# Optimization experiments

Measured on AMD Instinct MI355X. Metric: run time of the kernel, lower is better.

## Reference

```python
import jax, jax.numpy as jnp
import numpy as np

TOP_K = 2


def setup_inputs() -> dict:
    key = jax.random.key(0)
    ks = jax.random.split(key, 10)
    D, F, E = 1024, 4096, 8
    s = 0.02  # realistic init scale, keeps activations stable
    return {
        "x": jax.random.normal(ks[0], (2, 4096, D), dtype=jnp.float32),
        "gate_w": jax.random.normal(ks[1], (E, D), dtype=jnp.float32) * s,
        "w1": jax.random.normal(ks[2], (E, F, D), dtype=jnp.float32) * s,
        "b1": jax.random.normal(ks[3], (E, F), dtype=jnp.float32) * s,
        "w2": jax.random.normal(ks[4], (E, D, F), dtype=jnp.float32) * s,
        "b2": jax.random.normal(ks[5], (E, D), dtype=jnp.float32) * s,
        "sw1": jax.random.normal(ks[6], (F, D), dtype=jnp.float32) * s,
        "sb1": jax.random.normal(ks[7], (F,), dtype=jnp.float32) * s,
        "sw2": jax.random.normal(ks[8], (D, F), dtype=jnp.float32) * s,
        "sb2": jax.random.normal(ks[9], (D,), dtype=jnp.float32) * s,
    }


def _ffn(x, w1, b1, w2, b2):
    # GELU(x @ W1^T + b1) @ W2^T + b2 ; torch F.gelu default = exact (erf)
    h = jax.nn.gelu(x @ w1.T + b1, approximate=False)
    return h @ w2.T + b2


def reference(x, gate_w, w1, b1, w2, b2, sw1, sb1, sw2, sb2):
    B, S, D = x.shape
    E = gate_w.shape[0]
    xt = x.reshape(-1, D)  # [T, D]

    # MoEGate: linear -> softmax -> top-k (weights not renormalized)
    scores = jax.nn.softmax(xt @ gate_w.T, axis=-1)  # [T, E]
    topk_w, topk_idx = jax.lax.top_k(scores, TOP_K)  # [T, K]

    # moe_infer: per-expert FFN, combine with top-k gate weights.
    # Reference form: dense per-expert compute, masked combine (combine sum is
    # permutation-invariant so top-k ordering does not matter).
    out = jnp.zeros_like(xt)
    for e in range(E):
        we = jnp.sum(jnp.where(topk_idx == e, topk_w, 0.0), axis=-1)  # [T]
        out = out + we[:, None] * _ffn(xt, w1[e], b1[e], w2[e], b2[e])

    # shared expert applied to the identity input
    out = out + _ffn(xt, sw1, sb1, sw2, sb2)
    return out.reshape(B, S, D)
```

## Files before the change

### kernel.cpp

```cpp
#include <hip/hip_runtime.h>
#include <hip/hip_bf16.h>

typedef __bf16 bf16_t;
typedef __bf16 bf16x8 __attribute__((ext_vector_type(8)));
typedef float  f32x4  __attribute__((ext_vector_type(4)));

static constexpr int TT = 8192;
static constexpr int DD = 1024;
static constexpr int FF = 4096;
static constexpr int NSLOT = 2 * TT;

#define R_COUNTS 0
#define R_OFFSET 8
#define R_TSTART 17
#define R_TOTAL  34
#define R_INTS   40

#define GLL(g, l) __builtin_amdgcn_global_load_lds( \
    (__attribute__((address_space(1))) void*)(g), \
    (__attribute__((address_space(3))) void*)(l), 16, 0, 0)

__device__ __forceinline__ float fast_gelu(float v) {
  float t = -1.5957691216f * v - 0.0713548162f * (v * v * v);
  return v / (1.f + __expf(t));
}

__global__ __launch_bounds__(256) void cvt_f32_bf16(const float* __restrict__ src,
                                                    bf16_t* __restrict__ dst, int n8) {
  int i = blockIdx.x * 256 + threadIdx.x;
  if (i >= n8) return;
  const float4* s = reinterpret_cast<const float4*>(src) + (size_t)i * 2;
  float4 a = s[0], b = s[1];
  bf16x8 v;
  v[0] = (bf16_t)a.x; v[1] = (bf16_t)a.y; v[2] = (bf16_t)a.z; v[3] = (bf16_t)a.w;
  v[4] = (bf16_t)b.x; v[5] = (bf16_t)b.y; v[6] = (bf16_t)b.z; v[7] = (bf16_t)b.w;
  *reinterpret_cast<bf16x8*>(dst + (size_t)i * 8) = v;
}

__global__ __launch_bounds__(256) void gate_kernel(const float* __restrict__ x,
                                                   const float* __restrict__ gw,
                                                   float* __restrict__ topkw,
                                                   int* __restrict__ slote) {
  int wid = threadIdx.x >> 6, lane = threadIdx.x & 63;
  int t = blockIdx.x * 4 + wid;
  const float4* xv = reinterpret_cast<const float4*>(x + (size_t)t * DD) + lane * 4;
  const float4* gv = reinterpret_cast<const float4*>(gw);
  float acc[8];
#pragma unroll
  for (int e = 0; e < 8; ++e) acc[e] = 0.f;
#pragma unroll
  for (int i = 0; i < 4; ++i) {
    float4 xi = xv[i];
#pragma unroll
    for (int e = 0; e < 8; ++e) {
      float4 g = gv[e * 256 + lane * 4 + i];
      acc[e] += xi.x * g.x + xi.y * g.y + xi.z * g.z + xi.w * g.w;
    }
  }
#pragma unroll
  for (int e = 0; e < 8; ++e)
    for (int off = 32; off; off >>= 1) acc[e] += __shfl_xor(acc[e], off, 64);
  if (lane == 0) {
    float m = acc[0];
#pragma unroll
    for (int e = 1; e < 8; ++e) m = fmaxf(m, acc[e]);
    float p[8], s = 0.f;
#pragma unroll
    for (int e = 0; e < 8; ++e) { p[e] = expf(acc[e] - m); s += p[e]; }
    float inv = 1.f / s;
#pragma unroll
    for (int e = 0; e < 8; ++e) p[e] *= inv;
    int e1 = 0; float b1v = p[0];
#pragma unroll
    for (int e = 1; e < 8; ++e) if (p[e] > b1v) { b1v = p[e]; e1 = e; }
    int e2 = -1; float b2v = -1.f;
#pragma unroll
    for (int e = 0; e < 8; ++e) if (e != e1 && p[e] > b2v) { b2v = p[e]; e2 = e; }
    topkw[2 * t] = b1v;  topkw[2 * t + 1] = b2v;
    slote[2 * t] = e1;   slote[2 * t + 1] = e2;
  }
}

__global__ __launch_bounds__(256) void hist_kernel(const int* __restrict__ slote,
                                                   int* __restrict__ routing) {
  __shared__ int red[256];
  const int e = blockIdx.x;
  const int t = threadIdx.x;
  int cnt = 0;
  for (int base = 0; base < NSLOT; base += 256)
    cnt += (slote[base + t] == e) ? 1 : 0;
  red[t] = cnt;
  __syncthreads();
  for (int s = 128; s; s >>= 1) {
    if (t < s) red[t] += red[t + s];
    __syncthreads();
  }
  if (t == 0) routing[R_COUNTS + e] = red[0];
}

__global__ void scan_kernel(int* __restrict__ routing) {
  int off = 0, tt = 0;
  for (int e = 0; e < 8; ++e) {
    routing[R_OFFSET + e] = off;
    routing[R_TSTART + e] = tt;
    int c = routing[R_COUNTS + e];
    off += c;
    tt += (c + 127) >> 7;
  }
  routing[R_OFFSET + 8] = off;
  routing[R_TSTART + 8] = tt;
  routing[R_TOTAL] = tt;
}

__global__ __launch_bounds__(256) void scatter_kernel(const int* __restrict__ slote,
                                                      const int* __restrict__ routing,
                                                      int* __restrict__ perm,
                                                      int* __restrict__ pos) {
  __shared__ int wtot[4];
  const int e = blockIdx.x;
  const int t = threadIdx.x;
  const int lane = t & 63, wid = t >> 6;
  int running = routing[R_OFFSET + e];
  for (int base = 0; base < NSLOT; base += 256) {
    int s = base + t;
    bool m = (slote[s] == e);
    unsigned long long mask = __ballot(m);
    int wrank = __popcll(mask & ((1ull << lane) - 1ull));
    if (lane == 0) wtot[wid] = __popcll(mask);
    __syncthreads();
    int wpre = 0;
#pragma unroll
    for (int w = 0; w < 4; ++w) if (w < wid) wpre += wtot[w];
    int tot = wtot[0] + wtot[1] + wtot[2] + wtot[3];
    if (m) {
      int pp = running + wpre + wrank;
      perm[pp] = s;
      pos[s] = pp;
    }
    running += tot;
    __syncthreads();
  }
}

__global__ __launch_bounds__(256) void combine_kernel(const float* __restrict__ slotbuf,
                                                      const int* __restrict__ pos,
                                                      const float* __restrict__ topkw,
                                                      float* __restrict__ out) {
  int idx = blockIdx.x * 256 + threadIdx.x;
  int t = idx >> 8;
  int c = (idx & 255) << 2;
  int p0 = pos[2 * t], p1 = pos[2 * t + 1];
  float w0 = topkw[2 * t], w1 = topkw[2 * t + 1];
  float4 o = *reinterpret_cast<const float4*>(&out[(size_t)t * DD + c]);
  float4 s0 = *reinterpret_cast<const float4*>(&slotbuf[(size_t)p0 * DD + c]);
  float4 s1 = *reinterpret_cast<const float4*>(&slotbuf[(size_t)p1 * DD + c]);
  o.x += w0 * s0.x + w1 * s1.x;
  o.y += w0 * s0.y + w1 * s1.y;
  o.z += w0 * s0.z + w1 * s1.z;
  o.w += w0 * s0.w + w1 * s1.w;
  *reinterpret_cast<float4*>(&out[(size_t)t * DD + c]) = o;
}

template <int MODE>
__global__ __launch_bounds__(256, 4) void gemm_kernel(
    const bf16_t* __restrict__ A, const bf16_t* __restrict__ Bw,
    const float* __restrict__ bias, bf16_t* __restrict__ Hout,
    float* __restrict__ out, const int* __restrict__ routing,
    const int* __restrict__ perm) {
  constexpr bool G1 = (MODE == 0 || MODE == 2);
  constexpr bool EXPERT = (MODE < 2);
  constexpr int K = G1 ? 1024 : 4096;
  constexpr int NTOT = G1 ? 4096 : 1024;
  constexpr int NT = NTOT / 128;
  constexpr int NKT = K / 64;
  constexpr int OUTD = G1 ? FF : DD;

  __shared__ __align__(16) bf16_t lds[16384];

  const int t = threadIdx.x;
  const int lane = t & 63;
  const int wid = t >> 6;
  const int wm = wid >> 1;
  const int wn = wid & 1;

  const int nwg = gridDim.x;
  const int q = nwg >> 3, r = nwg & 7;
  const int xcd = blockIdx.x & 7, bi = blockIdx.x >> 3;
  const int swz = (xcd < r ? xcd * (q + 1) : r * (q + 1) + (xcd - r) * q) + bi;
  const int mt = swz / NT;
  const int nt = swz & (NT - 1);

  int row0, valid, eidx = 0;
  if constexpr (EXPERT) {
    if (mt >= routing[R_TOTAL]) return;
    int e = 0;
    while (e < 7 && routing[R_TSTART + e + 1] <= mt) ++e;
    eidx = e;
    int lm = mt - routing[R_TSTART + e];
    row0 = routing[R_OFFSET + e] + lm * 128;
    valid = min(128, routing[R_COUNTS + e] - lm * 128);
  } else {
    row0 = mt * 128;
    valid = 128;
  }

  const bf16_t* Bexp = Bw + (EXPERT ? (size_t)eidx * NTOT * K : 0);
  const float* biasp = bias + (EXPERT ? eidx * NTOT : 0);

  const int sub = t >> 3;
  const int lc = (t & 7) ^ (sub & 7);
  const bf16_t* aS[4];
  const bf16_t* bS[4];
#pragma unroll
  for (int i = 0; i < 4; ++i) {
    int lr = sub + i * 32;
    int gr;
    if constexpr (MODE == 0) {
      gr = perm[row0 + min(lr, valid - 1)] >> 1;
    } else if constexpr (MODE == 1) {
      gr = row0 + min(lr, valid - 1);
    } else {
      gr = row0 + lr;
    }
    aS[i] = A + (size_t)gr * K + lc * 8;
    bS[i] = Bexp + (size_t)(nt * 128 + lr) * K + lc * 8;
  }
  bf16_t* const aD = lds + (sub << 6) + ((t & 7) << 3);
  bf16_t* const bD = aD + 8192;

  const int l15 = lane & 15, lq = lane >> 4;

  f32x4 acc[4][4];
#pragma unroll
  for (int m = 0; m < 4; ++m)
#pragma unroll
    for (int n = 0; n < 4; ++n) acc[m][n] = f32x4{0.f, 0.f, 0.f, 0.f};

  for (int kt = 0; kt < NKT; ++kt) {
    const size_t kof = (size_t)kt * 64;
#pragma unroll
    for (int i = 0; i < 4; ++i) {
      GLL(aS[i] + kof, aD + i * 2048);
      GLL(bS[i] + kof, bD + i * 2048);
    }
    __syncthreads();

#pragma unroll
    for (int kk = 0; kk < 2; ++kk) {
      bf16x8 af[4], bfr[4];
#pragma unroll
      for (int m = 0; m < 4; ++m) {
        int ra = wm * 64 + m * 16 + l15;
        int ph = (kk * 4 + lq) ^ (ra & 7);
        af[m] = *reinterpret_cast<const bf16x8*>(&lds[ra * 64 + ph * 8]);
      }
#pragma unroll
      for (int n = 0; n < 4; ++n) {
        int rb = wn * 64 + n * 16 + l15;
        int ph = (kk * 4 + lq) ^ (rb & 7);
        bfr[n] = *reinterpret_cast<const bf16x8*>(&lds[8192 + rb * 64 + ph * 8]);
      }
      __builtin_amdgcn_s_setprio(1);
#pragma unroll
      for (int m = 0; m < 4; ++m)
#pragma unroll
        for (int n = 0; n < 4; ++n)
          acc[m][n] = __builtin_amdgcn_mfma_f32_16x16x32_bf16(af[m], bfr[n], acc[m][n], 0, 0, 0);
      __builtin_amdgcn_s_setprio(0);
    }
    __syncthreads();
  }

  float bc[4];
#pragma unroll
  for (int n = 0; n < 4; ++n) bc[n] = biasp[nt * 128 + wn * 64 + n * 16 + l15];

  if constexpr (G1) {
    bf16_t* scr = lds;
#pragma unroll
    for (int h = 0; h < 2; ++h) {
      __syncthreads();
      if (wm == h) {
#pragma unroll
        for (int m = 0; m < 4; ++m)
#pragma unroll
          for (int n = 0; n < 4; ++n)
#pragma unroll
            for (int rr = 0; rr < 4; ++rr) {
              float v = acc[m][n][rr] + bc[n];
              scr[(m * 16 + lq * 4 + rr) * 128 + wn * 64 + n * 16 + l15] = (bf16_t)fast_gelu(v);
            }
      }
      __syncthreads();
#pragma unroll
      for (int i = 0; i < 4; ++i) {
        int c = t + i * 256;
        int rowp = c >> 4, cc = c & 15;
        int lr = h * 64 + rowp;
        if (lr < valid) {
          bf16x8 v8 = *reinterpret_cast<const bf16x8*>(&scr[rowp * 128 + cc * 8]);
          *reinterpret_cast<bf16x8*>(&Hout[(size_t)(row0 + lr) * OUTD + nt * 128 + cc * 8]) = v8;
        }
      }
    }
  } else {
    float* scr = reinterpret_cast<float*>(lds);
#pragma unroll
    for (int h = 0; h < 2; ++h) {
      __syncthreads();
      if (wm == h) {
#pragma unroll
        for (int m = 0; m < 4; ++m)
#pragma unroll
          for (int n = 0; n < 4; ++n)
#pragma unroll
            for (int rr = 0; rr < 4; ++rr)
              scr[(m * 16 + lq * 4 + rr) * 128 + wn * 64 + n * 16 + l15] = acc[m][n][rr] + bc[n];
      }
      __syncthreads();
#pragma unroll
      for (int i = 0; i < 8; ++i) {
        int c = t + i * 256;
        int rowp = c >> 5, cc = c & 31;
        int lr = h * 64 + rowp;
        if (lr < valid) {
          float4 v4 = *reinterpret_cast<const float4*>(&scr[rowp * 128 + cc * 4]);
          *reinterpret_cast<float4*>(&out[(size_t)(row0 + lr) * OUTD + nt * 128 + cc * 4]) = v4;
        }
      }
    }
  }
}

extern "C" void kernel_launch(void* const* d_in, const int* in_sizes, int n_in,
                              void* d_out, int out_size, void* d_ws, size_t ws_size,
                              hipStream_t stream) {
  const float* x   = (const float*)d_in[0];
  const float* gw  = (const float*)d_in[1];
  const float* w1  = (const float*)d_in[2];
  const float* b1  = (const float*)d_in[3];
  const float* w2  = (const float*)d_in[4];
  const float* b2  = (const float*)d_in[5];
  const float* sw1 = (const float*)d_in[6];
  const float* sb1 = (const float*)d_in[7];
  const float* sw2 = (const float*)d_in[8];
  const float* sb2 = (const float*)d_in[9];
  float* out = (float*)d_out;

  char* ws = (char*)d_ws;
  bf16_t* xb    = (bf16_t*)(ws);
  bf16_t* w1b   = (bf16_t*)(ws + ((size_t)16 << 20));
  bf16_t* w2b   = (bf16_t*)(ws + ((size_t)80 << 20));
  bf16_t* sw1b  = (bf16_t*)(ws + ((size_t)144 << 20));
  bf16_t* sw2b  = (bf16_t*)(ws + ((size_t)152 << 20));
  bf16_t* Hbuf  = (bf16_t*)(ws + ((size_t)160 << 20));
  float*  slotbuf = (float*)(ws);
  float*  topkw = (float*)(ws + ((size_t)288 << 20));
  int*    slote = (int*)(ws + ((size_t)288 << 20) + 65536);
  int*    perm  = (int*)(ws + ((size_t)288 << 20) + 2 * 65536);
  int*    pos   = (int*)(ws + ((size_t)288 << 20) + 3 * 65536);
  int*    routing = (int*)(ws + ((size_t)288 << 20) + 4 * 65536);

  cvt_f32_bf16<<<(TT * DD / 8 + 255) / 256, 256, 0, stream>>>(x, xb, TT * DD / 8);
  cvt_f32_bf16<<<(8 * FF * DD / 8 + 255) / 256, 256, 0, stream>>>(w1, w1b, 8 * FF * DD / 8);
  cvt_f32_bf16<<<(8 * DD * FF / 8 + 255) / 256, 256, 0, stream>>>(w2, w2b, 8 * DD * FF / 8);
  cvt_f32_bf16<<<(FF * DD / 8 + 255) / 256, 256, 0, stream>>>(sw1, sw1b, FF * DD / 8);
  cvt_f32_bf16<<<(DD * FF / 8 + 255) / 256, 256, 0, stream>>>(sw2, sw2b, DD * FF / 8);

  gate_kernel<<<TT / 4, 256, 0, stream>>>(x, gw, topkw, slote);
  hist_kernel<<<8, 256, 0, stream>>>(slote, routing);
  scan_kernel<<<1, 1, 0, stream>>>(routing);
  scatter_kernel<<<8, 256, 0, stream>>>(slote, routing, perm, pos);

  gemm_kernel<2><<<64 * 32, 256, 0, stream>>>(xb, sw1b, sb1, Hbuf, out, routing, perm);
  gemm_kernel<3><<<64 * 8, 256, 0, stream>>>(Hbuf, sw2b, sb2, nullptr, out, routing, perm);
  gemm_kernel<0><<<136 * 32, 256, 0, stream>>>(xb, w1b, b1, Hbuf, out, routing, perm);
  gemm_kernel<1><<<136 * 8, 256, 0, stream>>>(Hbuf, w2b, b2, nullptr, slotbuf, routing, perm);

  combine_kernel<<<TT, 256, 0, stream>>>(slotbuf, pos, topkw, out);
}
```

Measured before the change: 709.8 us.

## Fuse x bf16 cast into gate, apply gate weights in expert GEMM epilogue, bf16 slot buffer

```diff
diff --git a/kernel.cpp b/kernel.cpp
--- a/kernel.cpp
+++ b/kernel.cpp
@@ -40,22 +40,35 @@
 __global__ __launch_bounds__(256) void gate_kernel(const float* __restrict__ x,
                                                    const float* __restrict__ gw,
                                                    float* __restrict__ topkw,
-                                                   int* __restrict__ slote) {
+                                                   int* __restrict__ slote,
+                                                   bf16_t* __restrict__ xb) {
   int wid = threadIdx.x >> 6, lane = threadIdx.x & 63;
   int t = blockIdx.x * 4 + wid;
   const float4* xv = reinterpret_cast<const float4*>(x + (size_t)t * DD) + lane * 4;
   const float4* gv = reinterpret_cast<const float4*>(gw);
   float acc[8];
+  float4 xs[4];
 #pragma unroll
   for (int e = 0; e < 8; ++e) acc[e] = 0.f;
 #pragma unroll
   for (int i = 0; i < 4; ++i) {
     float4 xi = xv[i];
+    xs[i] = xi;
 #pragma unroll
     for (int e = 0; e < 8; ++e) {
       float4 g = gv[e * 256 + lane * 4 + i];
       acc[e] += xi.x * g.x + xi.y * g.y + xi.z * g.z + xi.w * g.w;
     }
+  }
+  {
+    bf16x8 lo, hi;
+    lo[0]=(bf16_t)xs[0].x; lo[1]=(bf16_t)xs[0].y; lo[2]=(bf16_t)xs[0].z; lo[3]=(bf16_t)xs[0].w;
+    lo[4]=(bf16_t)xs[1].x; lo[5]=(bf16_t)xs[1].y; lo[6]=(bf16_t)xs[1].z; lo[7]=(bf16_t)xs[1].w;
+    hi[0]=(bf16_t)xs[2].x; hi[1]=(bf16_t)xs[2].y; hi[2]=(bf16_t)xs[2].z; hi[3]=(bf16_t)xs[2].w;
+    hi[4]=(bf16_t)xs[3].x; hi[5]=(bf16_t)xs[3].y; hi[6]=(bf16_t)xs[3].z; hi[7]=(bf16_t)xs[3].w;
+    bf16_t* d = xb + (size_t)t * DD + lane * 16;
+    *reinterpret_cast<bf16x8*>(d) = lo;
+    *reinterpret_cast<bf16x8*>(d + 8) = hi;
   }
 #pragma unroll
   for (int e = 0; e < 8; ++e)
@@ -142,23 +155,28 @@
   }
 }
 
-__global__ __launch_bounds__(256) void combine_kernel(const float* __restrict__ slotbuf,
+__global__ __launch_bounds__(256) void combine_kernel(const bf16_t* __restrict__ slotb,
                                                       const int* __restrict__ pos,
-                                                      const float* __restrict__ topkw,
                                                       float* __restrict__ out) {
   int idx = blockIdx.x * 256 + threadIdx.x;
-  int t = idx >> 8;
-  int c = (idx & 255) << 2;
+  int t = idx >> 7;
+  int c = (idx & 127) << 3;
   int p0 = pos[2 * t], p1 = pos[2 * t + 1];
-  float w0 = topkw[2 * t], w1 = topkw[2 * t + 1];
-  float4 o = *reinterpret_cast<const float4*>(&out[(size_t)t * DD + c]);
-  float4 s0 = *reinterpret_cast<const float4*>(&slotbuf[(size_t)p0 * DD + c]);
-  float4 s1 = *reinterpret_cast<const float4*>(&slotbuf[(size_t)p1 * DD + c]);
-  o.x += w0 * s0.x + w1 * s1.x;
-  o.y += w0 * s0.y + w1 * s1.y;
-  o.z += w0 * s0.z + w1 * s1.z;
-  o.w += w0 * s0.w + w1 * s1.w;
-  *reinterpret_cast<float4*>(&out[(size_t)t * DD + c]) = o;
+  bf16x8 s0 = *reinterpret_cast<const bf16x8*>(&slotb[(size_t)p0 * DD + c]);
+  bf16x8 s1 = *reinterpret_cast<const bf16x8*>(&slotb[(size_t)p1 * DD + c]);
+  float* o = &out[(size_t)t * DD + c];
+  float4 o0 = *reinterpret_cast<const float4*>(o);
+  float4 o1 = *reinterpret_cast<const float4*>(o + 4);
+  o0.x += (float)s0[0] + (float)s1[0];
+  o0.y += (float)s0[1] + (float)s1[1];
+  o0.z += (float)s0[2] + (float)s1[2];
+  o0.w += (float)s0[3] + (float)s1[3];
+  o1.x += (float)s0[4] + (float)s1[4];
+  o1.y += (float)s0[5] + (float)s1[5];
+  o1.z += (float)s0[6] + (float)s1[6];
+  o1.w += (float)s0[7] + (float)s1[7];
+  *reinterpret_cast<float4*>(o) = o0;
+  *reinterpret_cast<float4*>(o + 4) = o1;
 }
 
 template <int MODE>
@@ -166,16 +184,16 @@
     const bf16_t* __restrict__ A, const bf16_t* __restrict__ Bw,
     const float* __restrict__ bias, bf16_t* __restrict__ Hout,
     float* __restrict__ out, const int* __restrict__ routing,
-    const int* __restrict__ perm) {
-  constexpr bool G1 = (MODE == 0 || MODE == 2);
+    const int* __restrict__ perm, const float* __restrict__ topkw) {
   constexpr bool EXPERT = (MODE < 2);
-  constexpr int K = G1 ? 1024 : 4096;
-  constexpr int NTOT = G1 ? 4096 : 1024;
+  constexpr int K = (MODE == 0 || MODE == 2) ? 1024 : 4096;
+  constexpr int NTOT = (MODE == 0 || MODE == 2) ? 4096 : 1024;
   constexpr int NT = NTOT / 128;
   constexpr int NKT = K / 64;
-  constexpr int OUTD = G1 ? FF : DD;
+  constexpr int OUTD = (MODE == 0 || MODE == 2) ? FF : DD;
 
   __shared__ __align__(16) bf16_t lds[16384];
+  __shared__ float wrow[128];
 
   const int t = threadIdx.x;
   const int lane = t & 63;
@@ -271,11 +289,15 @@
     __syncthreads();
   }
 
+  if constexpr (MODE == 1) {
+    if (t < 128) wrow[t] = topkw[perm[row0 + min(t, valid - 1)]];
+  }
+
   float bc[4];
 #pragma unroll
   for (int n = 0; n < 4; ++n) bc[n] = biasp[nt * 128 + wn * 64 + n * 16 + l15];
 
-  if constexpr (G1) {
+  if constexpr (MODE != 3) {
     bf16_t* scr = lds;
 #pragma unroll
     for (int h = 0; h < 2; ++h) {
@@ -288,7 +310,10 @@
 #pragma unroll
             for (int rr = 0; rr < 4; ++rr) {
               float v = acc[m][n][rr] + bc[n];
-              scr[(m * 16 + lq * 4 + rr) * 128 + wn * 64 + n * 16 + l15] = (bf16_t)fast_gelu(v);
+              float o;
+              if constexpr (MODE == 1) o = wrow[h * 64 + m * 16 + lq * 4 + rr] * v;
+              else                     o = fast_gelu(v);
+              scr[(m * 16 + lq * 4 + rr) * 128 + wn * 64 + n * 16 + l15] = (bf16_t)o;
             }
       }
       __syncthreads();
@@ -323,10 +348,8 @@
         int c = t + i * 256;
         int rowp = c >> 5, cc = c & 31;
         int lr = h * 64 + rowp;
-        if (lr < valid) {
-          float4 v4 = *reinterpret_cast<const float4*>(&scr[rowp * 128 + cc * 4]);
-          *reinterpret_cast<float4*>(&out[(size_t)(row0 + lr) * OUTD + nt * 128 + cc * 4]) = v4;
-        }
+        float4 v4 = *reinterpret_cast<const float4*>(&scr[rowp * 128 + cc * 4]);
+        *reinterpret_cast<float4*>(&out[(size_t)(row0 + lr) * OUTD + nt * 128 + cc * 4]) = v4;
       }
     }
   }
@@ -354,28 +377,27 @@
   bf16_t* sw1b  = (bf16_t*)(ws + ((size_t)144 << 20));
   bf16_t* sw2b  = (bf16_t*)(ws + ((size_t)152 << 20));
   bf16_t* Hbuf  = (bf16_t*)(ws + ((size_t)160 << 20));
-  float*  slotbuf = (float*)(ws);
+  bf16_t* slotb = (bf16_t*)(ws);
   float*  topkw = (float*)(ws + ((size_t)288 << 20));
   int*    slote = (int*)(ws + ((size_t)288 << 20) + 65536);
   int*    perm  = (int*)(ws + ((size_t)288 << 20) + 2 * 65536);
   int*    pos   = (int*)(ws + ((size_t)288 << 20) + 3 * 65536);
   int*    routing = (int*)(ws + ((size_t)288 << 20) + 4 * 65536);
 
-  cvt_f32_bf16<<<(TT * DD / 8 + 255) / 256, 256, 0, stream>>>(x, xb, TT * DD / 8);
   cvt_f32_bf16<<<(8 * FF * DD / 8 + 255) / 256, 256, 0, stream>>>(w1, w1b, 8 * FF * DD / 8);
   cvt_f32_bf16<<<(8 * DD * FF / 8 + 255) / 256, 256, 0, stream>>>(w2, w2b, 8 * DD * FF / 8);
   cvt_f32_bf16<<<(FF * DD / 8 + 255) / 256, 256, 0, stream>>>(sw1, sw1b, FF * DD / 8);
   cvt_f32_bf16<<<(DD * FF / 8 + 255) / 256, 256, 0, stream>>>(sw2, sw2b, DD * FF / 8);
 
-  gate_kernel<<<TT / 4, 256, 0, stream>>>(x, gw, topkw, slote);
+  gate_kernel<<<TT / 4, 256, 0, stream>>>(x, gw, topkw, slote, xb);
   hist_kernel<<<8, 256, 0, stream>>>(slote, routing);
   scan_kernel<<<1, 1, 0, stream>>>(routing);
   scatter_kernel<<<8, 256, 0, stream>>>(slote, routing, perm, pos);
 
-  gemm_kernel<2><<<64 * 32, 256, 0, stream>>>(xb, sw1b, sb1, Hbuf, out, routing, perm);
-  gemm_kernel<3><<<64 * 8, 256, 0, stream>>>(Hbuf, sw2b, sb2, nullptr, out, routing, perm);
-  gemm_kernel<0><<<136 * 32, 256, 0, stream>>>(xb, w1b, b1, Hbuf, out, routing, perm);
-  gemm_kernel<1><<<136 * 8, 256, 0, stream>>>(Hbuf, w2b, b2, nullptr, slotbuf, routing, perm);
-
-  combine_kernel<<<TT, 256, 0, stream>>>(slotbuf, pos, topkw, out);
-}
+  gemm_kernel<2><<<64 * 32, 256, 0, stream>>>(xb, sw1b, sb1, Hbuf, out, routing, perm, nullptr);
+  gemm_kernel<3><<<64 * 8, 256, 0, stream>>>(Hbuf, sw2b, sb2, nullptr, out, routing, perm, nullptr);
+  gemm_kernel<0><<<136 * 32, 256, 0, stream>>>(xb, w1b, b1, Hbuf, out, routing, perm, nullptr);
+  gemm_kernel<1><<<136 * 8, 256, 0, stream>>>(Hbuf, w2b, b2, slotb, nullptr, routing, perm, topkw);
+
+  combine_kernel<<<TT * DD / 8 / 256, 256, 0, stream>>>(slotb, pos, out);
+}
```

After: 697.9 us. No clear change (-1.7%).
